# Optimization experiments

Measured on AMD Instinct MI355X. Metric: run time of the kernel, lower is better.

The kernel has to match this reference:

```python
import jax, jax.numpy as jnp
import numpy as np

C_IN = 512
OUT_CH = 256  # query/key gate channels
DIM = 64      # squeeze/extraction rank


def setup_inputs() -> dict:
    key = jax.random.key(0)
    ks = jax.random.split(key, 11)
    b, c, h, w = 16, C_IN, 64, 64

    def winit(k, o, i):
        # torch Conv2d default init: U(-s, s), s = 1/sqrt(fan_in)
        s = 1.0 / np.sqrt(i)
        return jax.random.uniform(k, (o, i), jnp.float32, -s, s)

    return {
        "x": jax.random.normal(ks[0], (b, c, h, w), jnp.float32),
        "Wq": winit(ks[1], OUT_CH, C_IN), "bq": winit(ks[2], OUT_CH, C_IN)[:, 0],
        "Wk": winit(ks[3], OUT_CH, C_IN), "bk": winit(ks[4], OUT_CH, C_IN)[:, 0],
        "Wv": winit(ks[5], C_IN, C_IN),   "bv": winit(ks[6], C_IN, C_IN)[:, 0],
        "Ws": winit(ks[7], DIM, C_IN),    "bs": winit(ks[8], DIM, C_IN)[:, 0],
        "We": winit(ks[9], DIM, C_IN),    "be": winit(ks[10], DIM, C_IN)[:, 0],
    }


def reference(x, Wq, bq, Wk, bk, Wv, bv, Ws, bs, We, be):
    b, c, h, w = x.shape
    n = h * w
    xf = x.reshape(b, c, n)  # [b, 512, n] (1x1 conv == matmul over channels)

    Q = jnp.einsum('oc,bcn->bon', Wq, xf) + bq[:, None]   # [b, 256, n]
    K = jnp.einsum('oc,bcn->bon', Wk, xf) + bk[:, None]   # [b, 256, n]
    gate = jax.nn.sigmoid(jnp.mean(Q * K, axis=1, keepdims=True))  # [b, 1, n]

    V = jnp.einsum('oc,bcn->bon', Wv, xf) + bv[:, None]   # [b, 512, n]
    V_dw = V * gate                                        # [b, 512, n]

    Qs = jnp.einsum('oc,bcn->bon', Ws, xf) + bs[:, None]   # [b, 64, n]
    Ke = jnp.einsum('oc,bcn->bon', We, xf) + be[:, None]   # [b, 64, n]

    energy = jnp.einsum('bcn,bdn->bcd', V_dw, Qs)           # [b, 512, 64]
    attention = jax.nn.softmax(energy, axis=-1)
    Vout = jnp.einsum('bcd,bdn->bcn', attention, Ke)        # [b, 512, n]

    return x + Vout.reshape(b, c, h, w)
```

## Files before the change

kernel.cpp:

```cpp
#include <hip/hip_runtime.h>

#define BATCH 16
#define CIN 512
#define NPIX 4096

typedef __attribute__((ext_vector_type(8))) short bf16x8;
typedef __attribute__((ext_vector_type(4))) float f32x4;

#define MFMA(a,b,c) __builtin_amdgcn_mfma_f32_16x16x32_bf16((a),(b),(c),0,0,0)

union PK  { short s[8]; bf16x8 v; };
union PK4 { short s[4]; uint2 u; };

__device__ __forceinline__ unsigned short bf16_rne(float f){
  unsigned u = __float_as_uint(f);
  return (unsigned short)((u + 0x7fffu + ((u >> 16) & 1u)) >> 16);
}
__device__ __forceinline__ void f32_split(float f, short &h, short &l){
  unsigned short hu = bf16_rne(f);
  h = (short)hu;
  float fh = __uint_as_float((unsigned)hu << 16);
  l = (short)bf16_rne(f - fh);
}
__device__ __forceinline__ void split8(float4 a, float4 b, bf16x8 &h, bf16x8 &l){
  float vv[8] = {a.x,a.y,a.z,a.w,b.x,b.y,b.z,b.w};
  PK ph, pl;
  #pragma unroll
  for (int z=0;z<8;z++){ short hh,ll; f32_split(vv[z],hh,ll); ph.s[z]=hh; pl.s[z]=ll; }
  h = ph.v; l = pl.v;
}

__device__ __forceinline__ int offBig(int row, int k){
  int s = k >> 3;
  s = (s & ~7) | ((s ^ row) & 7);
  return row*512 + s*8 + (k & 7);
}

__global__ __launch_bounds__(256)
void k_convw(const float* __restrict__ Wq, const float* __restrict__ bq,
             const float* __restrict__ Wk, const float* __restrict__ bk,
             const float* __restrict__ Ws, const float* __restrict__ bs,
             const float* __restrict__ We, const float* __restrict__ be,
             short* __restrict__ WG, short* __restrict__ WSE, short* __restrict__ WSL,
             float* __restrict__ BG, float* __restrict__ BSE){
  int t = blockIdx.x*256 + threadIdx.x;
  if (t < 512*512){
    int r = t >> 9, c = t & 511, o = r >> 1;
    float v = (r & 1) ? Wk[o*512+c] : Wq[o*512+c];
    WG[t] = (short)bf16_rne(v);
  }
  if (t < 128*512){
    int r = t >> 9, c = t & 511;
    float v = (r < 64) ? Ws[r*512+c] : We[(r-64)*512+c];
    short h,l; f32_split(v,h,l);
    WSE[t] = h;
    if (r < 64) WSL[t] = l;
  }
  if (t < 512) BG[t] = (t&1) ? bk[t>>1] : bq[t>>1];
  if (t < 128) BSE[t] = (t < 64) ? bs[t] : be[t-64];
}

__global__ __launch_bounds__(512)
void k_front(const float* __restrict__ x, const short* __restrict__ WG,
             const float* __restrict__ BG, const short* __restrict__ WSE,
             const short* __restrict__ WSL, const float* __restrict__ BSE,
             float* __restrict__ QSG, short* __restrict__ KET, float* __restrict__ S){
  __shared__ __align__(16) short XS[64*512];
  __shared__ float QKf[512];
  __shared__ float GF[64];
  int nt = blockIdx.x, b = blockIdx.y;
  int n0 = nt*64;
  int tid = threadIdx.x, w = tid>>6, lane = tid&63;
  int lr = lane&15, lk = (lane>>4)<<3;

  {
    const float* xp = x + ((size_t)b*CIN + tid)*NPIX + n0;
    for (int i=0;i<64;i+=4){
      float4 v = *(const float4*)(xp + i);
      float vv[4] = {v.x, v.y, v.z, v.w};
      #pragma unroll
      for (int u=0;u<4;u++)
        XS[offBig(i+u, tid)] = (short)bf16_rne(vv[u]);
    }
  }
  __syncthreads();

  {
    const short* wbase = WG + (size_t)(w*64 + lr)*512 + lk;
    f32x4 acc[4][4] = {};
    for (int kt=0; kt<16; kt++){
      bf16x8 av[4];
      #pragma unroll
      for (int r=0;r<4;r++) av[r] = *(const bf16x8*)(wbase + r*16*512 + kt*32);
      bf16x8 bb[4];
      #pragma unroll
      for (int j=0;j<4;j++) bb[j] = *(const bf16x8*)&XS[offBig(j*16+lr, kt*32+lk)];
      #pragma unroll
      for (int r=0;r<4;r++)
        #pragma unroll
        for (int j=0;j<4;j++)
          acc[r][j] = MFMA(av[r], bb[j], acc[r][j]);
    }
    float p[4] = {0.f,0.f,0.f,0.f};
    int rq = (lane>>4)<<2;
    #pragma unroll
    for (int r=0;r<4;r++){
      f32x4 bg = *(const f32x4*)&BG[w*64 + r*16 + rq];
      #pragma unroll
      for (int j=0;j<4;j++){
        f32x4 a4 = acc[r][j];
        p[j] += (a4[0]+bg[0])*(a4[1]+bg[1]) + (a4[2]+bg[2])*(a4[3]+bg[3]);
      }
    }
    #pragma unroll
    for (int j=0;j<4;j++){ p[j] += __shfl_xor(p[j],16); p[j] += __shfl_xor(p[j],32); }
    if (lane < 16){
      #pragma unroll
      for (int j=0;j<4;j++) QKf[w*64 + j*16 + lane] = p[j];
    }
  }
  __syncthreads();
  if (tid < 64){
    float s = 0.f;
    #pragma unroll
    for (int ww=0;ww<8;ww++) s += QKf[ww*64 + tid];
    GF[tid] = 1.f/(1.f + __expf(-s*(1.f/256.f)));
  }
  __syncthreads();

  bool isQs = (w < 4);
  int arow = isQs ? (w*16 + lr) : (64 + (w-4)*16 + lr);
  const short* wb  = WSE + (size_t)arow*512 + lk;
  const short* wlb = WSL + (size_t)(isQs ? (w*16 + lr) : 0)*512 + lk;
  f32x4 acc2[4] = {};
  for (int kt=0; kt<16; kt++){
    bf16x8 bb[4];
    #pragma unroll
    for (int j=0;j<4;j++) bb[j] = *(const bf16x8*)&XS[offBig(j*16+lr, kt*32+lk)];
    bf16x8 ah = *(const bf16x8*)(wb + kt*32);
    if (isQs){
      bf16x8 al = *(const bf16x8*)(wlb + kt*32);
      #pragma unroll
      for (int j=0;j<4;j++){
        acc2[j] = MFMA(al, bb[j], acc2[j]);
        acc2[j] = MFMA(ah, bb[j], acc2[j]);
      }
    } else {
      #pragma unroll
      for (int j=0;j<4;j++)
        acc2[j] = MFMA(ah, bb[j], acc2[j]);
    }
  }
  int rq = (lane>>4)<<2;
  if (isQs){
    int row0 = w*16 + rq;
    f32x4 bs4 = *(const f32x4*)&BSE[row0];
    float srow[4] = {0.f,0.f,0.f,0.f};
    #pragma unroll
    for (int j=0;j<4;j++){
      int nl = j*16 + lr;
      float g = GF[nl];
      int n = n0 + nl;
      #pragma unroll
      for (int q=0;q<4;q++){
        float v = (acc2[j][q] + bs4[q]) * g;
        QSG[((size_t)(b*64) + row0 + q)*NPIX + n] = v;
        srow[q] += v;
      }
    }
    #pragma unroll
    for (int q=0;q<4;q++){
      float v = srow[q];
      v += __shfl_xor(v,1); v += __shfl_xor(v,2);
      v += __shfl_xor(v,4); v += __shfl_xor(v,8);
      if (lr == 0) atomicAdd(&S[b*64 + row0 + q], v);
    }
  } else {
    int d0 = (w-4)*16 + rq;
    f32x4 be4 = *(const f32x4*)&BSE[64 + d0];
    #pragma unroll
    for (int j=0;j<4;j++){
      int n = n0 + j*16 + lr;
      PK4 pk;
      #pragma unroll
      for (int q=0;q<4;q++) pk.s[q] = (short)bf16_rne(acc2[j][q] + be4[q]);
      *(uint2*)&KET[((size_t)(b*NPIX) + n)*64 + d0] = pk.u;
    }
  }
}

__global__ __launch_bounds__(512)
void k_M(const float* __restrict__ x, const float* __restrict__ QSG,
         float* __restrict__ M){
  int slab = blockIdx.x, b = blockIdx.y;
  int tid = threadIdx.x, w = tid>>6, lane = tid&63;
  int lr = lane&15, lk8 = (lane>>4)<<3;
  f32x4 acc[4][4] = {};
  for (int kt=0; kt<8; kt++){
    int noff = slab*256 + kt*32 + lk8;
    bf16x8 bh[4], bl[4];
    #pragma unroll
    for (int j=0;j<4;j++){
      const float* qp = QSG + ((size_t)(b*64) + j*16 + lr)*NPIX + noff;
      split8(*(const float4*)qp, *(const float4*)(qp+4), bh[j], bl[j]);
    }
    #pragma unroll
    for (int r=0;r<4;r++){
      const float* xp = x + ((size_t)(b*CIN) + w*64 + r*16 + lr)*NPIX + noff;
      bf16x8 ah, al;
      split8(*(const float4*)xp, *(const float4*)(xp+4), ah, al);
      #pragma unroll
      for (int j=0;j<4;j++){
        acc[r][j] = MFMA(al, bh[j], acc[r][j]);
        acc[r][j] = MFMA(ah, bl[j], acc[r][j]);
        acc[r][j] = MFMA(ah, bh[j], acc[r][j]);
      }
    }
  }
  int rq = (lane>>4)<<2;
  #pragma unroll
  for (int r=0;r<4;r++)
    #pragma unroll
    for (int j=0;j<4;j++)
      #pragma unroll
      for (int q=0;q<4;q++)
        atomicAdd(&M[((size_t)(b*CIN) + w*64 + r*16 + rq + q)*64 + j*16 + lr], acc[r][j][q]);
}

__global__ __launch_bounds__(256)
void k_energy(const float* __restrict__ Wv, const float* __restrict__ bv,
              const float* __restrict__ M, const float* __restrict__ S,
              float* __restrict__ EN){
  __shared__ __align__(16) float ML[128*68];
  int cch = blockIdx.x, b = blockIdx.y;
  int tid = threadIdx.x;
  int d4 = tid & 15, ci = tid >> 4;
  f32x4 acc[2] = {};
  for (int kt=0; kt<4; kt++){
    __syncthreads();
    for (int i = tid; i < 2048; i += 256){
      int k = i >> 4, c4 = (i & 15) * 4;
      *(float4*)&ML[k*68 + c4] = *(const float4*)&M[((size_t)(b*CIN) + kt*128 + k)*64 + c4];
    }
    __syncthreads();
    #pragma unroll
    for (int m=0;m<2;m++){
      int c = cch*32 + ci + 16*m;
      const float* wvp = Wv + (size_t)c*512 + kt*128;
      for (int k4=0;k4<32;k4++){
        float4 wv4 = *(const float4*)(wvp + k4*4);
        f32x4 m0 = *(const f32x4*)&ML[(k4*4+0)*68 + d4*4];
        f32x4 m1 = *(const f32x4*)&ML[(k4*4+1)*68 + d4*4];
        f32x4 m2 = *(const f32x4*)&ML[(k4*4+2)*68 + d4*4];
        f32x4 m3 = *(const f32x4*)&ML[(k4*4+3)*68 + d4*4];
        acc[m] += m0*wv4.x + m1*wv4.y + m2*wv4.z + m3*wv4.w;
      }
    }
  }
  f32x4 s4 = *(const f32x4*)&S[b*64 + d4*4];
  #pragma unroll
  for (int m=0;m<2;m++){
    int c = cch*32 + ci + 16*m;
    f32x4 r = acc[m] + s4*bv[c];
    *(f32x4*)&EN[((size_t)(b*CIN) + c)*64 + d4*4] = r;
  }
}

__global__ __launch_bounds__(256)
void k_softmax(const float* __restrict__ EN, short* __restrict__ ATT){
  int row = blockIdx.x*4 + (threadIdx.x>>6);
  int lane = threadIdx.x & 63;
  float v = EN[(size_t)row*64 + lane];
  float m = v;
  #pragma unroll
  for (int s=1;s<64;s<<=1) m = fmaxf(m, __shfl_xor(m, s));
  float e = __expf(v - m);
  float sum = e;
  #pragma unroll
  for (int s=1;s<64;s<<=1) sum += __shfl_xor(sum, s);
  ATT[(size_t)row*64 + lane] = (short)bf16_rne(e / sum);
}

__global__ __launch_bounds__(512)
void k_out(const float* __restrict__ x, const short* __restrict__ ATT,
           const short* __restrict__ KET, float* __restrict__ out){
  int nt = blockIdx.x, b = blockIdx.y;
  int n0 = nt*64;
  int tid = threadIdx.x, w = tid>>6, lane = tid&63;
  int lr = lane&15, lk = (lane>>4)<<3;
  f32x4 acc[4][4] = {};
  #pragma unroll
  for (int kt=0; kt<2; kt++){
    bf16x8 bb[4];
    #pragma unroll
    for (int j=0;j<4;j++)
      bb[j] = *(const bf16x8*)&KET[((size_t)(b*NPIX) + n0 + j*16 + lr)*64 + kt*32 + lk];
    #pragma unroll
    for (int r=0;r<4;r++){
      bf16x8 a = *(const bf16x8*)&ATT[((size_t)(b*CIN) + w*64 + r*16 + lr)*64 + kt*32 + lk];
      #pragma unroll
      for (int j=0;j<4;j++)
        acc[r][j] = MFMA(a, bb[j], acc[r][j]);
    }
  }
  int rq = (lane>>4)<<2;
  #pragma unroll
  for (int r=0;r<4;r++)
    #pragma unroll
    for (int j=0;j<4;j++){
      int col = n0 + j*16 + lr;
      #pragma unroll
      for (int q=0;q<4;q++){
        size_t idx = ((size_t)(b*CIN) + w*64 + r*16 + rq + q)*NPIX + col;
        out[idx] = x[idx] + acc[r][j][q];
      }
    }
}

extern "C" void kernel_launch(void* const* d_in, const int* in_sizes, int n_in,
                              void* d_out, int out_size, void* d_ws, size_t ws_size,
                              hipStream_t stream){
  const float* x   = (const float*)d_in[0];
  const float* Wq  = (const float*)d_in[1];
  const float* bq  = (const float*)d_in[2];
  const float* Wk  = (const float*)d_in[3];
  const float* bk  = (const float*)d_in[4];
  const float* Wv  = (const float*)d_in[5];
  const float* bv  = (const float*)d_in[6];
  const float* Wsq = (const float*)d_in[7];
  const float* bsq = (const float*)d_in[8];
  const float* We  = (const float*)d_in[9];
  const float* be  = (const float*)d_in[10];
  float* out = (float*)d_out;

  char* wsb = (char*)d_ws;
  size_t off = 0;
  auto alloc = [&](size_t bytes)->void*{
    void* p = wsb + off; off += (bytes + 255) & ~(size_t)255; return p;
  };
  short* WG  = (short*)alloc((size_t)512*512*2);
  short* WSE = (short*)alloc((size_t)128*512*2);
  short* WSL = (short*)alloc((size_t)64*512*2);
  float* BG  = (float*)alloc(512*4);
  float* BSE = (float*)alloc(128*4);
  float* QSG = (float*)alloc((size_t)BATCH*64*NPIX*4);
  short* KET = (short*)alloc((size_t)BATCH*NPIX*64*2);
  float* Mb  = (float*)alloc((size_t)BATCH*512*64*4);
  float* Sb  = (float*)alloc((size_t)BATCH*64*4);
  float* EN  = (float*)alloc((size_t)BATCH*512*64*4);
  short* ATT = (short*)alloc((size_t)BATCH*512*64*2);

  hipMemsetAsync(Mb, 0, (size_t)BATCH*512*64*4, stream);
  hipMemsetAsync(Sb, 0, (size_t)BATCH*64*4, stream);

  k_convw  <<<1024, 256, 0, stream>>>(Wq,bq,Wk,bk,Wsq,bsq,We,be, WG,WSE,WSL,BG,BSE);
  k_front  <<<dim3(64,16), 512, 0, stream>>>(x, WG, BG, WSE, WSL, BSE, QSG, KET, Sb);
  k_M      <<<dim3(16,16), 512, 0, stream>>>(x, QSG, Mb);
  k_energy <<<dim3(16,16), 256, 0, stream>>>(Wv, bv, Mb, Sb, EN);
  k_softmax<<<2048, 256, 0, stream>>>(EN, ATT);
  k_out    <<<dim3(64,16), 512, 0, stream>>>(x, ATT, KET, out);
}
```

Before: 278.9 us.

## Halve k_front LDS via two-pass channel staging, pre-split QSG, double k_M grid

k_front now stages x into shared memory in two 256-channel halves instead of all 512 channels. This halves LDS use and lets the gate and Qs/Ke GEMMs share each staged tile; a launch-bounds min-blocks hint is added to raise occupancy. k_front also writes the gated Qs as pre-split bf16 hi/lo arrays, so k_M no longer reads fp32 and splits it on the fly. k_M covers half as many pixels per block with twice the blocks. The costs are extra register pressure from holding both accumulator sets, an extra barrier per half, and the loss of the reused x split when the two fused loops compete for registers.

```diff
diff --git a/kernel.cpp b/kernel.cpp
--- a/kernel.cpp
+++ b/kernel.cpp
@@ -28,12 +28,6 @@
   #pragma unroll
   for (int z=0;z<8;z++){ short hh,ll; f32_split(vv[z],hh,ll); ph.s[z]=hh; pl.s[z]=ll; }
   h = ph.v; l = pl.v;
-}
-
-__device__ __forceinline__ int offBig(int row, int k){
-  int s = k >> 3;
-  s = (s & ~7) | ((s ^ row) & 7);
-  return row*512 + s*8 + (k & 7);
 }
 
 __global__ __launch_bounds__(256)
@@ -60,55 +54,90 @@
   if (t < 128) BSE[t] = (t < 64) ? bs[t] : be[t-64];
 }
 
-__global__ __launch_bounds__(512)
+__global__ __launch_bounds__(512, 4)
 void k_front(const float* __restrict__ x, const short* __restrict__ WG,
              const float* __restrict__ BG, const short* __restrict__ WSE,
              const short* __restrict__ WSL, const float* __restrict__ BSE,
-             float* __restrict__ QSG, short* __restrict__ KET, float* __restrict__ S){
-  __shared__ __align__(16) short XS[64*512];
+             short* __restrict__ QSGH, short* __restrict__ QSGL,
+             short* __restrict__ KET, float* __restrict__ S){
+  __shared__ __align__(16) short XS[64*256];
   __shared__ float QKf[512];
   __shared__ float GF[64];
   int nt = blockIdx.x, b = blockIdx.y;
   int n0 = nt*64;
   int tid = threadIdx.x, w = tid>>6, lane = tid&63;
   int lr = lane&15, lk = (lane>>4)<<3;
-
-  {
-    const float* xp = x + ((size_t)b*CIN + tid)*NPIX + n0;
-    for (int i=0;i<64;i+=4){
-      float4 v = *(const float4*)(xp + i);
-      float vv[4] = {v.x, v.y, v.z, v.w};
-      #pragma unroll
-      for (int u=0;u<4;u++)
-        XS[offBig(i+u, tid)] = (short)bf16_rne(vv[u]);
-    }
-  }
-  __syncthreads();
-
-  {
-    const short* wbase = WG + (size_t)(w*64 + lr)*512 + lk;
-    f32x4 acc[4][4] = {};
-    for (int kt=0; kt<16; kt++){
-      bf16x8 av[4];
-      #pragma unroll
-      for (int r=0;r<4;r++) av[r] = *(const bf16x8*)(wbase + r*16*512 + kt*32);
+  bool isQs = (w < 4);
+  const short* wgb = WG  + (size_t)(w*64 + lr)*512 + lk;
+  const short* wb  = WSE + (size_t)((isQs ? (w*16) : (64 + (w-4)*16)) + lr)*512 + lk;
+  const short* wlb = WSL + (size_t)((isQs ? (w*16) : 0) + lr)*512 + lk;
+
+  f32x4 acc1[4][4] = {};
+  f32x4 acc2[4] = {};
+  int cl = tid & 255, nh = tid >> 8;
+  int sbase = cl >> 3, clo = cl & 7;
+
+  for (int half=0; half<2; half++){
+    __syncthreads();
+    {
+      const float* xp = x + ((size_t)(b*CIN) + half*256 + cl)*NPIX + n0 + nh*32;
+      #pragma unroll
+      for (int u=0;u<32;u+=4){
+        float4 v = *(const float4*)(xp + u);
+        float vv[4] = {v.x,v.y,v.z,v.w};
+        #pragma unroll
+        for (int z=0;z<4;z++){
+          int row = nh*32 + u + z;
+          int s = (sbase & ~7) | ((sbase ^ row) & 7);
+          XS[row*256 + s*8 + clo] = (short)bf16_rne(vv[z]);
+        }
+      }
+    }
+    __syncthreads();
+    int kg = half*256;
+    for (int kt=0; kt<8; kt++){
       bf16x8 bb[4];
       #pragma unroll
-      for (int j=0;j<4;j++) bb[j] = *(const bf16x8*)&XS[offBig(j*16+lr, kt*32+lk)];
-      #pragma unroll
-      for (int r=0;r<4;r++)
+      for (int j=0;j<4;j++){
+        int row = j*16 + lr;
+        int s = (kt*32 + lk) >> 3;
+        s = (s & ~7) | ((s ^ row) & 7);
+        bb[j] = *(const bf16x8*)&XS[row*256 + s*8];
+      }
+      {
+        bf16x8 ah = *(const bf16x8*)(wb + kg + kt*32);
+        if (isQs){
+          bf16x8 al = *(const bf16x8*)(wlb + kg + kt*32);
+          #pragma unroll
+          for (int j=0;j<4;j++){
+            acc2[j] = MFMA(al, bb[j], acc2[j]);
+            acc2[j] = MFMA(ah, bb[j], acc2[j]);
+          }
+        } else {
+          #pragma unroll
+          for (int j=0;j<4;j++)
+            acc2[j] = MFMA(ah, bb[j], acc2[j]);
+        }
+      }
+      #pragma unroll
+      for (int r=0;r<4;r++){
+        bf16x8 av = *(const bf16x8*)(wgb + (size_t)(r*16)*512 + kg + kt*32);
         #pragma unroll
         for (int j=0;j<4;j++)
-          acc[r][j] = MFMA(av[r], bb[j], acc[r][j]);
-    }
+          acc1[r][j] = MFMA(av, bb[j], acc1[r][j]);
+      }
+    }
+  }
+
+  int rq = (lane>>4)<<2;
+  {
     float p[4] = {0.f,0.f,0.f,0.f};
-    int rq = (lane>>4)<<2;
     #pragma unroll
     for (int r=0;r<4;r++){
       f32x4 bg = *(const f32x4*)&BG[w*64 + r*16 + rq];
       #pragma unroll
       for (int j=0;j<4;j++){
-        f32x4 a4 = acc[r][j];
+        f32x4 a4 = acc1[r][j];
         p[j] += (a4[0]+bg[0])*(a4[1]+bg[1]) + (a4[2]+bg[2])*(a4[3]+bg[3]);
       }
     }
@@ -128,30 +157,6 @@
   }
   __syncthreads();
 
-  bool isQs = (w < 4);
-  int arow = isQs ? (w*16 + lr) : (64 + (w-4)*16 + lr);
-  const short* wb  = WSE + (size_t)arow*512 + lk;
-  const short* wlb = WSL + (size_t)(isQs ? (w*16 + lr) : 0)*512 + lk;
-  f32x4 acc2[4] = {};
-  for (int kt=0; kt<16; kt++){
-    bf16x8 bb[4];
-    #pragma unroll
-    for (int j=0;j<4;j++) bb[j] = *(const bf16x8*)&XS[offBig(j*16+lr, kt*32+lk)];
-    bf16x8 ah = *(const bf16x8*)(wb + kt*32);
-    if (isQs){
-      bf16x8 al = *(const bf16x8*)(wlb + kt*32);
-      #pragma unroll
-      for (int j=0;j<4;j++){
-        acc2[j] = MFMA(al, bb[j], acc2[j]);
-        acc2[j] = MFMA(ah, bb[j], acc2[j]);
-      }
-    } else {
-      #pragma unroll
-      for (int j=0;j<4;j++)
-        acc2[j] = MFMA(ah, bb[j], acc2[j]);
-    }
-  }
-  int rq = (lane>>4)<<2;
   if (isQs){
     int row0 = w*16 + rq;
     f32x4 bs4 = *(const f32x4*)&BSE[row0];
@@ -164,7 +169,9 @@
       #pragma unroll
       for (int q=0;q<4;q++){
         float v = (acc2[j][q] + bs4[q]) * g;
-        QSG[((size_t)(b*64) + row0 + q)*NPIX + n] = v;
+        short h,l; f32_split(v,h,l);
+        QSGH[((size_t)(b*64) + row0 + q)*NPIX + n] = h;
+        QSGL[((size_t)(b*64) + row0 + q)*NPIX + n] = l;
         srow[q] += v;
       }
     }
@@ -190,19 +197,19 @@
 }
 
 __global__ __launch_bounds__(512)
-void k_M(const float* __restrict__ x, const float* __restrict__ QSG,
-         float* __restrict__ M){
+void k_M(const float* __restrict__ x, const short* __restrict__ QSGH,
+         const short* __restrict__ QSGL, float* __restrict__ M){
   int slab = blockIdx.x, b = blockIdx.y;
   int tid = threadIdx.x, w = tid>>6, lane = tid&63;
   int lr = lane&15, lk8 = (lane>>4)<<3;
   f32x4 acc[4][4] = {};
-  for (int kt=0; kt<8; kt++){
-    int noff = slab*256 + kt*32 + lk8;
+  for (int kt=0; kt<4; kt++){
+    int noff = slab*128 + kt*32 + lk8;
     bf16x8 bh[4], bl[4];
     #pragma unroll
     for (int j=0;j<4;j++){
-      const float* qp = QSG + ((size_t)(b*64) + j*16 + lr)*NPIX + noff;
-      split8(*(const float4*)qp, *(const float4*)(qp+4), bh[j], bl[j]);
+      bh[j] = *(const bf16x8*)&QSGH[((size_t)(b*64) + j*16 + lr)*NPIX + noff];
+      bl[j] = *(const bf16x8*)&QSGL[((size_t)(b*64) + j*16 + lr)*NPIX + noff];
     }
     #pragma unroll
     for (int r=0;r<4;r++){
@@ -338,24 +345,25 @@
   auto alloc = [&](size_t bytes)->void*{
     void* p = wsb + off; off += (bytes + 255) & ~(size_t)255; return p;
   };
-  short* WG  = (short*)alloc((size_t)512*512*2);
-  short* WSE = (short*)alloc((size_t)128*512*2);
-  short* WSL = (short*)alloc((size_t)64*512*2);
-  float* BG  = (float*)alloc(512*4);
-  float* BSE = (float*)alloc(128*4);
-  float* QSG = (float*)alloc((size_t)BATCH*64*NPIX*4);
-  short* KET = (short*)alloc((size_t)BATCH*NPIX*64*2);
-  float* Mb  = (float*)alloc((size_t)BATCH*512*64*4);
-  float* Sb  = (float*)alloc((size_t)BATCH*64*4);
-  float* EN  = (float*)alloc((size_t)BATCH*512*64*4);
-  short* ATT = (short*)alloc((size_t)BATCH*512*64*2);
+  short* WG   = (short*)alloc((size_t)512*512*2);
+  short* WSE  = (short*)alloc((size_t)128*512*2);
+  short* WSL  = (short*)alloc((size_t)64*512*2);
+  float* BG   = (float*)alloc(512*4);
+  float* BSE  = (float*)alloc(128*4);
+  short* QSGH = (short*)alloc((size_t)BATCH*64*NPIX*2);
+  short* QSGL = (short*)alloc((size_t)BATCH*64*NPIX*2);
+  short* KET  = (short*)alloc((size_t)BATCH*NPIX*64*2);
+  float* Mb   = (float*)alloc((size_t)BATCH*512*64*4);
+  float* Sb   = (float*)alloc((size_t)BATCH*64*4);
+  float* EN   = (float*)alloc((size_t)BATCH*512*64*4);
+  short* ATT  = (short*)alloc((size_t)BATCH*512*64*2);
 
   hipMemsetAsync(Mb, 0, (size_t)BATCH*512*64*4, stream);
   hipMemsetAsync(Sb, 0, (size_t)BATCH*64*4, stream);
 
   k_convw  <<<1024, 256, 0, stream>>>(Wq,bq,Wk,bk,Wsq,bsq,We,be, WG,WSE,WSL,BG,BSE);
-  k_front  <<<dim3(64,16), 512, 0, stream>>>(x, WG, BG, WSE, WSL, BSE, QSG, KET, Sb);
-  k_M      <<<dim3(16,16), 512, 0, stream>>>(x, QSG, Mb);
+  k_front  <<<dim3(64,16), 512, 0, stream>>>(x, WG, BG, WSE, WSL, BSE, QSGH, QSGL, KET, Sb);
+  k_M      <<<dim3(32,16), 512, 0, stream>>>(x, QSGH, QSGL, Mb);
   k_energy <<<dim3(16,16), 256, 0, stream>>>(Wv, bv, Mb, Sb, EN);
   k_softmax<<<2048, 256, 0, stream>>>(EN, ATT);
   k_out    <<<dim3(64,16), 512, 0, stream>>>(x, ATT, KET, out);
```

Result: slower. 371.9 us (+33.4%).
